# Optimization experiments

Hardware: AMD Instinct MI355X
Metric: run time of the kernel (lower is better)

The kernel has to match this reference:

```python
import jax, jax.numpy as jnp
import numpy as np

TOP_K = 4

def setup_inputs() -> dict:
    key = jax.random.key(0)
    ks = jax.random.split(key, 10)
    s = 0.02
    return {
        "x": jax.random.normal(ks[0], (4, 1024, 2048), jnp.float32),
        "expert_bias": jnp.zeros((64,), jnp.float32),
        "router_w": jax.random.normal(ks[1], (64, 2048), jnp.float32) * s,
        "gate_w": jax.random.normal(ks[2], (8192, 2048), jnp.float32) * s,
        "up_w": jax.random.normal(ks[3], (8192, 2048), jnp.float32) * s,
        "down_w": jax.random.normal(ks[4], (2048, 8192), jnp.float32) * s,
        "w_down": jax.random.normal(ks[5], (512, 2048), jnp.float32) * s,
        "w_up": jax.random.normal(ks[6], (2048, 512), jnp.float32) * s,
        "experts_w12": jax.random.normal(ks[7], (64, 512, 2048), jnp.float32) * s,
        "experts_w3": jax.random.normal(ks[8], (64, 1024, 512), jnp.float32) * s,
    }


def reference(x, expert_bias, router_w, gate_w, up_w, down_w, w_down, w_up, experts_w12, experts_w3):
    B, S, D = x.shape
    E = router_w.shape[0]
    K = TOP_K
    h = x.reshape(-1, D)            # [N, D]
    N = h.shape[0]
    NK = N * K

    # --- router (fp32) ---
    logits = h @ router_w.T          # [N, E]
    scores = jax.nn.sigmoid(logits)
    z_loss = jnp.mean(logits * logits) * 1e-4
    sel = scores + expert_bias
    _, topk_idx = jax.lax.top_k(sel, K)                      # [N, K]
    topk_logits = jnp.take_along_axis(logits, topk_idx, axis=1)
    gating = jax.nn.softmax(topk_logits, axis=-1)            # [N, K]

    # --- shared SwiGLU expert ---
    shared = (jax.nn.silu(h @ gate_w.T) * (h @ up_w.T)) @ down_w.T   # [N, D]

    # --- bottleneck down projection ---
    hd = h @ w_down.T                # [N, bottle]
    Bn = hd.shape[1]

    # --- dispatch: sort tokens by expert, capacity max_load per expert ---
    flat = topk_idx.reshape(-1)                      # [NK]
    perm = jnp.argsort(flat)                         # stable sort
    sorted_e = flat[perm]
    counts = jnp.bincount(flat, length=E)
    ptr = jnp.cumsum(counts) - counts                # start offset per expert
    local = jnp.arange(NK) - ptr[sorted_e]           # rank within expert
    max_load = (NK // E // 8 + 6) * 8                # static python int
    num_slots = E * max_load
    mask = local < max_load
    slots = sorted_e * max_load + local
    tok = jnp.repeat(jnp.arange(N), K)               # token id per routed slot

    # reverse_map[slot] = token index (N = dummy)
    rm = jnp.full((num_slots + 1,), N, dtype=jnp.int32)
    rm = rm.at[jnp.where(mask, slots, num_slots)].set(tok[perm].astype(jnp.int32))
    reverse_map = rm[:num_slots]

    hwd = jnp.concatenate([hd, jnp.zeros((1, Bn), hd.dtype)], axis=0)
    padding = hwd[reverse_map].reshape(E, max_load, Bn)

    # --- grouped expert GEMMs ---
    h12 = jnp.einsum('emb,ebf->emf', padding, experts_w12)   # [E, L, 2*F]
    h1, h2 = jnp.split(h12, 2, axis=-1)
    pout = jnp.einsum('emf,efb->emb', jax.nn.silu(h1) * h2, experts_w3)
    pout = pout.reshape(-1, Bn)                              # [num_slots, bottle]

    # --- combine: gather back per (token, k) slot and mix with gating ---
    powd = jnp.concatenate([pout, jnp.zeros((1, Bn), pout.dtype)], axis=0)
    gm = jnp.full((NK + 1,), num_slots, dtype=jnp.int32)
    gm = gm.at[jnp.where(mask, perm, NK)].set(jnp.where(mask, slots, num_slots).astype(jnp.int32))
    gather_map = gm[:NK]
    gathered = powd[gather_map].reshape(N, K, Bn)
    routed_b = jnp.einsum('nk,nkb->nb', gating, gathered)
    routed = routed_b @ w_up.T                               # [N, D]

    # eval mode: route_scale = 1.0, moe_scale = 0.5 (one shared expert), aux_loss = 0
    out = (shared + routed) * 0.5
    return out.reshape(B, S, D), z_loss
```

## Files before the change

### kernel.cpp

```cpp
#include <hip/hip_runtime.h>
#include <math.h>

#define NTOK 4096
#define DMODEL 2048
#define ENUM 64
#define HSH 8192
#define BND 512
#define FEXP 1024
#define MAXL 304
#define EPAD 384
#define ECH 16

typedef float f32x4 __attribute__((ext_vector_type(4)));
using bf16x8 = __attribute__((ext_vector_type(8))) __bf16;

typedef const __attribute__((address_space(1))) unsigned int cgu32;
typedef __attribute__((address_space(3))) unsigned int lu32;
#define GLOAD16(g, l) __builtin_amdgcn_global_load_lds((cgu32*)(g), (lu32*)(l), 16, 0, 0)

__device__ __forceinline__ unsigned short f2bf(float f) {
    union { float f; unsigned int u; } v; v.f = f;
    unsigned int u = v.u;
    return (unsigned short)((u + 0x7FFFu + ((u >> 16) & 1u)) >> 16);
}
__device__ __forceinline__ float bf2f(unsigned short s) {
    union { unsigned int u; float f; } v; v.u = ((unsigned int)s) << 16;
    return v.f;
}

__global__ __launch_bounds__(256) void init_kernel(float* zacc, int* slot2tok, unsigned short* hdz) {
    int i = blockIdx.x * 256 + threadIdx.x;
    if (i == 0) *zacc = 0.f;
    if (i < ENUM * MAXL) slot2tok[i] = NTOK;
    if (i < BND) hdz[i] = 0;
}

__global__ __launch_bounds__(256) void convert_kernel(
    const float* __restrict__ in, unsigned short* __restrict__ out, long long n)
{
    long long stride = (long long)gridDim.x * 256 * 8;
    for (long long i = ((long long)blockIdx.x * 256 + threadIdx.x) * 8; i < n; i += stride) {
        float4 a = *(const float4*)(in + i);
        float4 b = *(const float4*)(in + i + 4);
        union { unsigned short s[8]; uint4 v; } o;
        o.s[0] = f2bf(a.x); o.s[1] = f2bf(a.y); o.s[2] = f2bf(a.z); o.s[3] = f2bf(a.w);
        o.s[4] = f2bf(b.x); o.s[5] = f2bf(b.y); o.s[6] = f2bf(b.z); o.s[7] = f2bf(b.w);
        *(uint4*)(out + i) = o.v;
    }
}

__global__ __launch_bounds__(256) void convert_x_kernel(
    const float* __restrict__ in, unsigned short* __restrict__ hi,
    unsigned short* __restrict__ lo, long long n)
{
    long long stride = (long long)gridDim.x * 256 * 8;
    for (long long i = ((long long)blockIdx.x * 256 + threadIdx.x) * 8; i < n; i += stride) {
        float4 a = *(const float4*)(in + i);
        float4 b = *(const float4*)(in + i + 4);
        union { unsigned short s[8]; uint4 v; } oh, ol;
        float f[8] = {a.x, a.y, a.z, a.w, b.x, b.y, b.z, b.w};
#pragma unroll
        for (int j = 0; j < 8; j++) {
            unsigned short h = f2bf(f[j]);
            oh.s[j] = h;
            ol.s[j] = f2bf(f[j] - bf2f(h));
        }
        *(uint4*)(hi + i) = oh.v;
        *(uint4*)(lo + i) = ol.v;
    }
}

__global__ __launch_bounds__(256) void convert_rw_kernel(
    const float* __restrict__ rw, unsigned short* __restrict__ whi,
    unsigned short* __restrict__ wlo)
{
    int i = (blockIdx.x * 256 + threadIdx.x) * 4;
    if (i >= 128 * 2048) return;
    ushort4 oh = {0, 0, 0, 0}, ol = {0, 0, 0, 0};
    if (i < 64 * 2048) {
        float4 f = *(const float4*)(rw + i);
        float v[4] = {f.x, f.y, f.z, f.w};
        unsigned short h;
        h = f2bf(v[0]); oh.x = h; ol.x = f2bf(v[0] - bf2f(h));
        h = f2bf(v[1]); oh.y = h; ol.y = f2bf(v[1] - bf2f(h));
        h = f2bf(v[2]); oh.z = h; ol.z = f2bf(v[2] - bf2f(h));
        h = f2bf(v[3]); oh.w = h; ol.w = f2bf(v[3] - bf2f(h));
    }
    *(ushort4*)(whi + i) = oh;
    *(ushort4*)(wlo + i) = ol;
}

__global__ __launch_bounds__(256) void tconv_kernel(
    const float* __restrict__ in, unsigned short* __restrict__ out, int Kd, int Nd)
{
    __shared__ float t[32][33];
    size_t zoff = (size_t)blockIdx.z * Kd * Nd;
    in += zoff; out += zoff;
    int n0 = blockIdx.x * 32, k0 = blockIdx.y * 32;
    int r = threadIdx.x >> 3, c = (threadIdx.x & 7) * 4;
    float4 v = *(const float4*)(in + (size_t)(k0 + r) * Nd + n0 + c);
    t[r][c] = v.x; t[r][c + 1] = v.y; t[r][c + 2] = v.z; t[r][c + 3] = v.w;
    __syncthreads();
    ushort4 o;
    o.x = f2bf(t[c + 0][r]); o.y = f2bf(t[c + 1][r]);
    o.z = f2bf(t[c + 2][r]); o.w = f2bf(t[c + 3][r]);
    *(ushort4*)(out + (size_t)(n0 + r) * Kd + k0 + c) = o;
}

__global__ __launch_bounds__(256) void rgemm_kernel(
    const unsigned short* __restrict__ xb, const unsigned short* __restrict__ xlo,
    const unsigned short* __restrict__ whi, const unsigned short* __restrict__ wlo,
    float* __restrict__ logits)
{
    __shared__ unsigned short As[2][128 * 64];
    __shared__ unsigned short Bs[2][128 * 64];
    const int z = blockIdx.z;
    const int m0 = blockIdx.y * 128;
    const int tid = threadIdx.x;
    const int lane = tid & 63;
    const int w = tid >> 6;
    const int wm = (w >> 1) * 64;
    const int wn = (w & 1) * 64;

    const unsigned short* Ab = (z == 2) ? xlo : xb;
    const unsigned short* Bb = (z == 1) ? wlo : whi;
    float* Cb = logits + (size_t)z * NTOK * 128;

    size_t asrc[4], bsrc[4];
    int ldso[4];
#pragma unroll
    for (int i = 0; i < 4; i++) {
        int u = i * 256 + tid;
        int r = u >> 3;
        int ce = ((u & 7) ^ (r & 7)) * 8;
        ldso[i] = u * 8;
        asrc[i] = (size_t)(m0 + r) * DMODEL + ce;
        bsrc[i] = (size_t)r * DMODEL + ce;
    }

    const int lrow = lane & 15;
    const int kg = lane >> 4;
    const int mk = (lrow & 7) << 4;
    int arx[4], brx[4];
#pragma unroll
    for (int t = 0; t < 4; t++) {
        arx[t] = (wm + t * 16 + lrow) * 128;
        brx[t] = (wn + t * 16 + lrow) * 128;
    }

    f32x4 acc[4][4];
#pragma unroll
    for (int a = 0; a < 4; a++)
#pragma unroll
        for (int b = 0; b < 4; b++) acc[a][b] = (f32x4)0.f;

#pragma unroll
    for (int i = 0; i < 4; i++) GLOAD16(Ab + asrc[i], &As[0][ldso[i]]);
#pragma unroll
    for (int i = 0; i < 4; i++) GLOAD16(Bb + bsrc[i], &Bs[0][ldso[i]]);
#pragma unroll
    for (int i = 0; i < 4; i++) GLOAD16(Ab + asrc[i] + 64, &As[1][ldso[i]]);
#pragma unroll
    for (int i = 0; i < 4; i++) GLOAD16(Bb + bsrc[i] + 64, &Bs[1][ldso[i]]);

    const int nt = DMODEL >> 6;
    int cur = 0;
    for (int t = 0; t < nt; ++t) {
        if (t + 1 < nt) asm volatile("s_waitcnt vmcnt(8)" ::: "memory");
        else            asm volatile("s_waitcnt vmcnt(0)" ::: "memory");
        __builtin_amdgcn_s_barrier();
        __builtin_amdgcn_sched_barrier(0);
        const char* Abase = (const char*)&As[cur][0];
        const char* Bbase = (const char*)&Bs[cur][0];
#pragma unroll
        for (int ks = 0; ks < 2; ks++) {
            const int cb = (ks * 64 + kg * 16) ^ mk;
            bf16x8 a[4], b[4];
#pragma unroll
            for (int t2 = 0; t2 < 4; t2++) {
                a[t2] = *(const bf16x8*)(Abase + arx[t2] + cb);
                b[t2] = *(const bf16x8*)(Bbase + brx[t2] + cb);
            }
#pragma unroll
            for (int ni = 0; ni < 4; ni++)
#pragma unroll
                for (int mi = 0; mi < 4; mi++)
                    acc[mi][ni] = __builtin_amdgcn_mfma_f32_16x16x32_bf16(a[mi], b[ni], acc[mi][ni], 0, 0, 0);
        }
        __builtin_amdgcn_sched_barrier(0);
        asm volatile("s_waitcnt lgkmcnt(0)" ::: "memory");
        __builtin_amdgcn_s_barrier();
        __builtin_amdgcn_sched_barrier(0);
        const int kn = (t + 2) * 64;
        if (kn < DMODEL) {
#pragma unroll
            for (int i = 0; i < 4; i++) GLOAD16(Ab + asrc[i] + kn, &As[cur][ldso[i]]);
#pragma unroll
            for (int i = 0; i < 4; i++) GLOAD16(Bb + bsrc[i] + kn, &Bs[cur][ldso[i]]);
        }
        cur ^= 1;
    }

    const int rb0 = m0 + wm + (kg << 2);
#pragma unroll
    for (int mi = 0; mi < 4; mi++)
#pragma unroll
        for (int ni = 0; ni < 4; ni++) {
            int col = wn + ni * 16 + lrow;
#pragma unroll
            for (int r = 0; r < 4; r++)
                Cb[(size_t)(rb0 + mi * 16 + r) * 128 + col] = acc[mi][ni][r];
        }
}

__global__ __launch_bounds__(256) void topk_kernel(
    const float* __restrict__ logits, const float* __restrict__ bias,
    int* __restrict__ topk_idx, float* __restrict__ gating, float* __restrict__ zacc)
{
    __shared__ float zpart[4];
    const size_t Z = (size_t)NTOK * 128;
    int wv = threadIdx.x >> 6, lane = threadIdx.x & 63;
    int n = blockIdx.x * 4 + wv;
    const float* lp = logits + (size_t)n * 128 + lane;
    float logit = lp[0] + lp[Z] + lp[2 * Z];
    float sel = 1.f / (1.f + expf(-logit)) + bias[lane];
    float zsq = logit * logit;
    for (int off = 32; off; off >>= 1) zsq += __shfl_down(zsq, off);
    if (lane == 0) zpart[wv] = zsq;
    __syncthreads();
    if (threadIdx.x == 0) atomicAdd(zacc, zpart[0] + zpart[1] + zpart[2] + zpart[3]);
    float cur = sel;
    float ch_logit[4]; int ch_idx[4];
    for (int kk = 0; kk < 4; kk++) {
        float v = cur; int idx = lane;
        for (int off = 1; off < 64; off <<= 1) {
            float v2 = __shfl_xor(v, off);
            int i2 = __shfl_xor(idx, off);
            if (v2 > v || (v2 == v && i2 < idx)) { v = v2; idx = i2; }
        }
        ch_idx[kk] = idx;
        ch_logit[kk] = __shfl(logit, idx);
        if (lane == idx) cur = -1e30f;
    }
    if (lane == 0) {
        float mx = ch_logit[0];
        for (int kk = 1; kk < 4; kk++) mx = fmaxf(mx, ch_logit[kk]);
        float se = 0.f, ex[4];
        for (int kk = 0; kk < 4; kk++) { ex[kk] = expf(ch_logit[kk] - mx); se += ex[kk]; }
        for (int kk = 0; kk < 4; kk++) {
            topk_idx[n * 4 + kk] = ch_idx[kk];
            gating[n * 4 + kk] = ex[kk] / se;
        }
    }
}

__global__ __launch_bounds__(256) void rank_kernel(
    const int* __restrict__ topk_idx, int* __restrict__ slot2tok, int* __restrict__ gmap)
{
    int e = blockIdx.x;
    __shared__ int wsum[4];
    int tid = threadIdx.x;
    int lane = tid & 63, w = tid >> 6;
    int running = 0;
    for (int c = 0; c < NTOK * 4; c += 256) {
        int i = c + tid;
        int fl = topk_idx[i];
        bool m = (fl == e);
        unsigned long long bal = __ballot(m);
        int prefix = __popcll(bal & ((1ULL << lane) - 1ULL));
        if (lane == 0) wsum[w] = __popcll(bal);
        __syncthreads();
        int wbase = 0;
        for (int j = 0; j < w; j++) wbase += wsum[j];
        int total = wsum[0] + wsum[1] + wsum[2] + wsum[3];
        if (m) {
            int rank = running + wbase + prefix;
            int tok = i >> 2;
            if (rank < MAXL) {
                slot2tok[e * MAXL + rank] = tok;
                gmap[i] = e * MAXL + rank;
            } else gmap[i] = -1;
        }
        running += total;
        __syncthreads();
    }
}

template<int GATHER, int EPI>
__global__ __launch_bounds__(256) void gemm2(
    const unsigned short* __restrict__ A, long long aZ, int lda,
    const int* __restrict__ gtab,
    const unsigned short* __restrict__ Bm, long long bZ, int ldb,
    void* __restrict__ Cb, long long cZ, int ldc,
    int M, int K)
{
    __shared__ unsigned short As[2][128 * 64];
    __shared__ unsigned short Bs[2][128 * 64];
    const int z = blockIdx.z;
    const int m0 = blockIdx.y * 128;
    const int n0 = blockIdx.x * 128;
    const int tid = threadIdx.x;
    const int lane = tid & 63;
    const int w = tid >> 6;
    const int wm = (w >> 1) * 64;
    const int wn = (w & 1) * 64;

    const unsigned short* Ab = A + (GATHER ? (size_t)0 : (size_t)z * aZ);
    const unsigned short* Bb = Bm + (size_t)z * bZ;

    size_t asrc[4], bsrc[4];
    int ldso[4];
#pragma unroll
    for (int i = 0; i < 4; i++) {
        int u = i * 256 + tid;
        int r = u >> 3;
        int ce = ((u & 7) ^ (r & 7)) * 8;
        ldso[i] = u * 8;
        if constexpr (GATHER) {
            int mr = m0 + r;
            int tok = (mr < M) ? gtab[(size_t)z * MAXL + mr] : NTOK;
            asrc[i] = (size_t)tok * lda + ce;
        } else {
            asrc[i] = (size_t)(m0 + r) * lda + ce;
        }
        bsrc[i] = (size_t)(n0 + r) * ldb + ce;
    }

    const int lrow = lane & 15;
    const int kg = lane >> 4;
    const int mk = (lrow & 7) << 4;
    int arx[4], brx[4];
#pragma unroll
    for (int t = 0; t < 4; t++) {
        arx[t] = (wm + t * 16 + lrow) * 128;
        brx[t] = (wn + t * 16 + lrow) * 128;
    }

    f32x4 acc[4][4];
#pragma unroll
    for (int a = 0; a < 4; a++)
#pragma unroll
        for (int b = 0; b < 4; b++) acc[a][b] = (f32x4)0.f;

#pragma unroll
    for (int i = 0; i < 4; i++) GLOAD16(Ab + asrc[i], &As[0][ldso[i]]);
#pragma unroll
    for (int i = 0; i < 4; i++) GLOAD16(Bb + bsrc[i], &Bs[0][ldso[i]]);
    if (64 < K) {
#pragma unroll
        for (int i = 0; i < 4; i++) GLOAD16(Ab + asrc[i] + 64, &As[1][ldso[i]]);
#pragma unroll
        for (int i = 0; i < 4; i++) GLOAD16(Bb + bsrc[i] + 64, &Bs[1][ldso[i]]);
    }

    const int nt = K >> 6;
    int cur = 0;
    for (int t = 0; t < nt; ++t) {
        if (t + 1 < nt) asm volatile("s_waitcnt vmcnt(8)" ::: "memory");
        else            asm volatile("s_waitcnt vmcnt(0)" ::: "memory");
        __builtin_amdgcn_s_barrier();
        __builtin_amdgcn_sched_barrier(0);
        const char* Abase = (const char*)&As[cur][0];
        const char* Bbase = (const char*)&Bs[cur][0];
#pragma unroll
        for (int ks = 0; ks < 2; ks++) {
            const int cb = (ks * 64 + kg * 16) ^ mk;
            bf16x8 a[4], b[4];
#pragma unroll
            for (int t2 = 0; t2 < 4; t2++) {
                a[t2] = *(const bf16x8*)(Abase + arx[t2] + cb);
                b[t2] = *(const bf16x8*)(Bbase + brx[t2] + cb);
            }
#pragma unroll
            for (int ni = 0; ni < 4; ni++)
#pragma unroll
                for (int mi = 0; mi < 4; mi++)
                    acc[mi][ni] = __builtin_amdgcn_mfma_f32_16x16x32_bf16(a[mi], b[ni], acc[mi][ni], 0, 0, 0);
        }
        __builtin_amdgcn_sched_barrier(0);
        asm volatile("s_waitcnt lgkmcnt(0)" ::: "memory");
        __builtin_amdgcn_s_barrier();
        __builtin_amdgcn_sched_barrier(0);
        const int kn = (t + 2) * 64;
        if (kn < K) {
#pragma unroll
            for (int i = 0; i < 4; i++) GLOAD16(Ab + asrc[i] + kn, &As[cur][ldso[i]]);
#pragma unroll
            for (int i = 0; i < 4; i++) GLOAD16(Bb + bsrc[i] + kn, &Bs[cur][ldso[i]]);
        }
        cur ^= 1;
    }

    const int rb0 = m0 + wm + (kg << 2);
#pragma unroll
    for (int mi = 0; mi < 4; mi++)
#pragma unroll
        for (int ni = 0; ni < 4; ni++) {
            int col = n0 + wn + ni * 16 + lrow;
#pragma unroll
            for (int r = 0; r < 4; r++) {
                int row = rb0 + mi * 16 + r;
                if (row < M) {
                    size_t ci = (size_t)z * cZ + (size_t)row * ldc + col;
                    float v = acc[mi][ni][r];
                    if constexpr (EPI == 0) {
                        ((unsigned short*)Cb)[ci] = f2bf(v);
                    } else if constexpr (EPI == 1) {
                        unsigned short* cp = (unsigned short*)Cb + ci;
                        float g = bf2f(*cp);
                        *cp = f2bf(g / (1.f + expf(-g)) * v);
                    } else if constexpr (EPI == 2) {
                        ((float*)Cb)[ci] = v;
                    } else {
                        float* cp = (float*)Cb + ci;
                        *cp = (*cp + v) * 0.5f;
                    }
                }
            }
        }
}

template<int EPI>
__global__ __launch_bounds__(512) void gemm3(
    const unsigned short* __restrict__ A, int lda,
    const unsigned short* __restrict__ Bm, int ldb,
    unsigned short* __restrict__ C, int ldc, int K)
{
    __shared__ unsigned short As[3][256 * 32];
    __shared__ unsigned short Bs[3][256 * 32];
    const int m0 = blockIdx.y * 256;
    const int n0 = blockIdx.x * 256;
    const int tid = threadIdx.x;
    const int lane = tid & 63;
    const int w = tid >> 6;
    const int wm = (w >> 2) * 128;
    const int wn = (w & 3) * 64;

    size_t asrc[2], bsrc[2];
    int ldso[2];
#pragma unroll
    for (int i = 0; i < 2; i++) {
        int u = i * 512 + tid;
        int r = u >> 2;
        int ce = ((u & 3) ^ ((r >> 1) & 3)) * 8;
        ldso[i] = u * 8;
        asrc[i] = (size_t)(m0 + r) * lda + ce;
        bsrc[i] = (size_t)(n0 + r) * ldb + ce;
    }

    const int lrow = lane & 15;
    const int kg = lane >> 4;
    const int un = (kg ^ ((lrow >> 1) & 3)) << 4;
    int arx[8], brx[4];
#pragma unroll
    for (int mi = 0; mi < 8; mi++) arx[mi] = (wm + mi * 16 + lrow) * 64 + un;
#pragma unroll
    for (int ni = 0; ni < 4; ni++) brx[ni] = (wn + ni * 16 + lrow) * 64 + un;

    f32x4 acc[8][4];
#pragma unroll
    for (int a = 0; a < 8; a++)
#pragma unroll
        for (int b = 0; b < 4; b++) acc[a][b] = (f32x4)0.f;

#pragma unroll
    for (int i = 0; i < 2; i++) GLOAD16(A + asrc[i], &As[0][ldso[i]]);
#pragma unroll
    for (int i = 0; i < 2; i++) GLOAD16(Bm + bsrc[i], &Bs[0][ldso[i]]);
#pragma unroll
    for (int i = 0; i < 2; i++) GLOAD16(A + asrc[i] + 32, &As[1][ldso[i]]);
#pragma unroll
    for (int i = 0; i < 2; i++) GLOAD16(Bm + bsrc[i] + 32, &Bs[1][ldso[i]]);

    const int nt = K >> 5;
    int cur = 0;
    for (int t = 0; t < nt; ++t) {
        if (t + 1 < nt) asm volatile("s_waitcnt vmcnt(4)" ::: "memory");
        else            asm volatile("s_waitcnt vmcnt(0)" ::: "memory");
        __builtin_amdgcn_s_barrier();
        __builtin_amdgcn_sched_barrier(0);
        if (t + 2 < nt) {
            int nb = cur + 2; if (nb >= 3) nb -= 3;
            const int kn = (t + 2) * 32;
#pragma unroll
            for (int i = 0; i < 2; i++) GLOAD16(A + asrc[i] + kn, &As[nb][ldso[i]]);
#pragma unroll
            for (int i = 0; i < 2; i++) GLOAD16(Bm + bsrc[i] + kn, &Bs[nb][ldso[i]]);
        }
        const char* Abase = (const char*)&As[cur][0];
        const char* Bbase = (const char*)&Bs[cur][0];
        bf16x8 a[8], b[4];
#pragma unroll
        for (int mi = 0; mi < 8; mi++) a[mi] = *(const bf16x8*)(Abase + arx[mi]);
#pragma unroll
        for (int ni = 0; ni < 4; ni++) b[ni] = *(const bf16x8*)(Bbase + brx[ni]);
        __builtin_amdgcn_s_setprio(1);
#pragma unroll
        for (int ni = 0; ni < 4; ni++)
#pragma unroll
            for (int mi = 0; mi < 8; mi++)
                acc[mi][ni] = __builtin_amdgcn_mfma_f32_16x16x32_bf16(a[mi], b[ni], acc[mi][ni], 0, 0, 0);
        __builtin_amdgcn_s_setprio(0);
        __builtin_amdgcn_sched_barrier(0);
        asm volatile("s_waitcnt lgkmcnt(0)" ::: "memory");
        __builtin_amdgcn_s_barrier();
        __builtin_amdgcn_sched_barrier(0);
        cur += 1; if (cur >= 3) cur -= 3;
    }

    const int rb0 = m0 + wm + (kg << 2);
#pragma unroll
    for (int mi = 0; mi < 8; mi++)
#pragma unroll
        for (int ni = 0; ni < 4; ni++) {
            int col = n0 + wn + ni * 16 + lrow;
#pragma unroll
            for (int r = 0; r < 4; r++) {
                int row = rb0 + mi * 16 + r;
                size_t ci = (size_t)row * ldc + col;
                float v = acc[mi][ni][r];
                if constexpr (EPI == 0) {
                    C[ci] = f2bf(v);
                } else {
                    unsigned short* cp = C + ci;
                    float g = bf2f(*cp);
                    *cp = f2bf(g / (1.f + expf(-g)) * v);
                }
            }
        }
}

__global__ __launch_bounds__(256) void siluact_kernel(
    const unsigned short* __restrict__ h12, unsigned short* __restrict__ act)
{
    int e = blockIdx.y, m = blockIdx.x;
    const unsigned short* hr = h12 + ((size_t)e * EPAD + m) * 2048;
    unsigned short* ar = act + ((size_t)e * EPAD + m) * 1024;
    int j = threadIdx.x * 4;
    ushort4 h1 = *(const ushort4*)(hr + j);
    ushort4 h2 = *(const ushort4*)(hr + 1024 + j);
    ushort4 o;
    float v;
    v = bf2f(h1.x); o.x = f2bf(v / (1.f + expf(-v)) * bf2f(h2.x));
    v = bf2f(h1.y); o.y = f2bf(v / (1.f + expf(-v)) * bf2f(h2.y));
    v = bf2f(h1.z); o.z = f2bf(v / (1.f + expf(-v)) * bf2f(h2.z));
    v = bf2f(h1.w); o.w = f2bf(v / (1.f + expf(-v)) * bf2f(h2.w));
    *(ushort4*)(ar + j) = o;
}

__global__ __launch_bounds__(256) void gather_kernel(
    const unsigned short* __restrict__ pout, const int* __restrict__ gmap,
    const float* __restrict__ gating, unsigned short* __restrict__ routed_b)
{
    int n = blockIdx.x;
    int j = threadIdx.x * 2;
    float a0 = 0.f, a1 = 0.f;
#pragma unroll
    for (int kk = 0; kk < 4; kk++) {
        int slot = gmap[n * 4 + kk];
        float g = gating[n * 4 + kk];
        if (slot >= 0) {
            const unsigned short* pr = pout + (size_t)slot * BND + j;
            a0 += g * bf2f(pr[0]);
            a1 += g * bf2f(pr[1]);
        }
    }
    routed_b[(size_t)n * BND + j] = f2bf(a0);
    routed_b[(size_t)n * BND + j + 1] = f2bf(a1);
}

__global__ void zloss_kernel(const float* zacc, float* out) {
    out[0] = zacc[0] * (1.0e-4f / (float)(NTOK * ENUM));
}

extern "C" void kernel_launch(void* const* d_in, const int* in_sizes, int n_in,
                              void* d_out, int out_size, void* d_ws, size_t ws_size,
                              hipStream_t stream)
{
    const float* x      = (const float*)d_in[0];
    const float* ebias  = (const float*)d_in[1];
    const float* rw     = (const float*)d_in[2];
    const float* gate_w = (const float*)d_in[3];
    const float* up_w   = (const float*)d_in[4];
    const float* down_w = (const float*)d_in[5];
    const float* w_down = (const float*)d_in[6];
    const float* w_up   = (const float*)d_in[7];
    const float* w12    = (const float*)d_in[8];
    const float* w3     = (const float*)d_in[9];
    float* out = (float*)d_out;

    char* ws = (char*)d_ws;
    size_t off = 0;
    auto alloc = [&](size_t b) { size_t o = off; off += (b + 255) & ~(size_t)255; return o; };
    float* zacc     = (float*)(ws + alloc(4));
    int*   topk     = (int*)(ws + alloc((size_t)NTOK * 4 * 4));
    float* gating   = (float*)(ws + alloc((size_t)NTOK * 4 * 4));
    int*   gmap     = (int*)(ws + alloc((size_t)NTOK * 4 * 4));
    int*   slot2tok = (int*)(ws + alloc((size_t)ENUM * MAXL * 4));
    unsigned short* xb     = (unsigned short*)(ws + alloc((size_t)NTOK * DMODEL * 2));
    unsigned short* hd     = (unsigned short*)(ws + alloc((size_t)(NTOK + 1) * BND * 2));
    unsigned short* rb     = (unsigned short*)(ws + alloc((size_t)NTOK * BND * 2));
    unsigned short* wdownb = (unsigned short*)(ws + alloc((size_t)BND * DMODEL * 2));
    unsigned short* wupb   = (unsigned short*)(ws + alloc((size_t)DMODEL * BND * 2));
    unsigned short* wbuf   = (unsigned short*)(ws + alloc((size_t)HSH * DMODEL * 2));
    unsigned short* H1     = (unsigned short*)(ws + alloc((size_t)NTOK * HSH * 2));
    unsigned short* h12  = H1;
    unsigned short* act  = H1 + (size_t)ECH * EPAD * 2048;
    unsigned short* pout = H1 + (size_t)ECH * EPAD * 2048 + (size_t)ECH * EPAD * 1024;
    unsigned short* xlo    = H1;
    float*          logits = (float*)((char*)H1 + (size_t)NTOK * DMODEL * 2);
    unsigned short* whi    = (unsigned short*)((char*)logits + (size_t)3 * NTOK * 128 * 4);
    unsigned short* wlo    = whi + (size_t)128 * DMODEL;

    init_kernel<<<(ENUM * MAXL + 255) / 256, 256, 0, stream>>>(zacc, slot2tok, hd + (size_t)NTOK * BND);

    convert_x_kernel<<<1024, 256, 0, stream>>>(x, xb, xlo, (long long)NTOK * DMODEL);
    convert_rw_kernel<<<(128 * 2048 / 4 + 255) / 256, 256, 0, stream>>>(rw, whi, wlo);
    rgemm_kernel<<<dim3(1, NTOK / 128, 3), 256, 0, stream>>>(xb, xlo, whi, wlo, logits);
    topk_kernel<<<NTOK / 4, 256, 0, stream>>>(logits, ebias, topk, gating, zacc);
    rank_kernel<<<ENUM, 256, 0, stream>>>(topk, slot2tok, gmap);

    convert_kernel<<<256, 256, 0, stream>>>(w_down, wdownb, (long long)BND * DMODEL);
    convert_kernel<<<256, 256, 0, stream>>>(w_up, wupb, (long long)DMODEL * BND);

    gemm2<0, 0><<<dim3(BND / 128, NTOK / 128, 1), 256, 0, stream>>>(
        xb, 0, DMODEL, nullptr, wdownb, 0, DMODEL, hd, 0, BND, NTOK, DMODEL);

    convert_kernel<<<1024, 256, 0, stream>>>(gate_w, wbuf, (long long)HSH * DMODEL);
    gemm3<0><<<dim3(HSH / 256, NTOK / 256), 512, 0, stream>>>(
        xb, DMODEL, wbuf, DMODEL, H1, HSH, DMODEL);
    convert_kernel<<<1024, 256, 0, stream>>>(up_w, wbuf, (long long)HSH * DMODEL);
    gemm3<1><<<dim3(HSH / 256, NTOK / 256), 512, 0, stream>>>(
        xb, DMODEL, wbuf, DMODEL, H1, HSH, DMODEL);
    convert_kernel<<<1024, 256, 0, stream>>>(down_w, wbuf, (long long)DMODEL * HSH);
    gemm2<0, 2><<<dim3(DMODEL / 128, NTOK / 128, 1), 256, 0, stream>>>(
        H1, 0, HSH, nullptr, wbuf, 0, HSH, out, 0, DMODEL, NTOK, HSH);

    for (int c = 0; c < ENUM / ECH; c++) {
        tconv_kernel<<<dim3(2048 / 32, 512 / 32, ECH), 256, 0, stream>>>(
            w12 + (size_t)c * ECH * 512 * 2048, wbuf, 512, 2048);
        gemm2<1, 0><<<dim3(2048 / 128, 3, ECH), 256, 0, stream>>>(
            hd, 0, BND, slot2tok + (size_t)c * ECH * MAXL,
            wbuf, (long long)2048 * 512, 512,
            h12, (long long)EPAD * 2048, 2048, MAXL, BND);
        tconv_kernel<<<dim3(512 / 32, 1024 / 32, ECH), 256, 0, stream>>>(
            w3 + (size_t)c * ECH * 1024 * 512, wbuf, 1024, 512);
        siluact_kernel<<<dim3(EPAD, ECH), 256, 0, stream>>>(h12, act);
        gemm2<0, 0><<<dim3(BND / 128, 3, ECH), 256, 0, stream>>>(
            act, (long long)EPAD * FEXP, FEXP, nullptr,
            wbuf, (long long)BND * FEXP, FEXP,
            pout + (size_t)c * ECH * MAXL * BND, (long long)MAXL * BND, BND, MAXL, FEXP);
    }

    gather_kernel<<<NTOK, 256, 0, stream>>>(pout, gmap, gating, rb);

    gemm2<0, 3><<<dim3(DMODEL / 128, NTOK / 128, 1), 256, 0, stream>>>(
        rb, 0, BND, nullptr, wupb, 0, BND, out, 0, DMODEL, NTOK, BND);

    zloss_kernel<<<1, 1, 0, stream>>>(zacc, out + (size_t)NTOK * DMODEL);
}
```

Baseline: 1.124 ms.

## Deepen shared-GEMM pipeline to 4 stages and interleave prefetch with MFMA phases

The 256x256 bf16 GEMM used for the shared expert's gate and up projections moves from a 3-buffer to a 4-buffer LDS ring, prefetching three K-tiles ahead. The second end-of-iteration barrier is removed, and the A fragment loads and global prefetches are split into four phases that are interleaved with the MFMA groups. The aim is to hide global-load latency and shorten barrier stalls. In exchange, LDS use per block grows to 128KB, which limits occupancy to one block per CU. There is also a possible WAR hazard, because prefetches into slot (kt+3)&3 now rely on only one barrier per iteration.

```diff
diff --git a/kernel.cpp b/kernel.cpp
--- a/kernel.cpp
+++ b/kernel.cpp
@@ -421,13 +421,13 @@
 }
 
 template<int EPI>
-__global__ __launch_bounds__(512) void gemm3(
+__global__ __launch_bounds__(512) void gemm4(
     const unsigned short* __restrict__ A, int lda,
     const unsigned short* __restrict__ Bm, int ldb,
     unsigned short* __restrict__ C, int ldc, int K)
 {
-    __shared__ unsigned short As[3][256 * 32];
-    __shared__ unsigned short Bs[3][256 * 32];
+    __shared__ unsigned short As[4][256 * 32];
+    __shared__ unsigned short Bs[4][256 * 32];
     const int m0 = blockIdx.y * 256;
     const int n0 = blockIdx.x * 256;
     const int tid = threadIdx.x;
@@ -463,49 +463,54 @@
 #pragma unroll
         for (int b = 0; b < 4; b++) acc[a][b] = (f32x4)0.f;
 
-#pragma unroll
-    for (int i = 0; i < 2; i++) GLOAD16(A + asrc[i], &As[0][ldso[i]]);
-#pragma unroll
-    for (int i = 0; i < 2; i++) GLOAD16(Bm + bsrc[i], &Bs[0][ldso[i]]);
-#pragma unroll
-    for (int i = 0; i < 2; i++) GLOAD16(A + asrc[i] + 32, &As[1][ldso[i]]);
-#pragma unroll
-    for (int i = 0; i < 2; i++) GLOAD16(Bm + bsrc[i] + 32, &Bs[1][ldso[i]]);
-
-    const int nt = K >> 5;
-    int cur = 0;
-    for (int t = 0; t < nt; ++t) {
-        if (t + 1 < nt) asm volatile("s_waitcnt vmcnt(4)" ::: "memory");
-        else            asm volatile("s_waitcnt vmcnt(0)" ::: "memory");
+    const int NT = K >> 5;
+    for (int t = 0; t < 3 && t < NT; ++t) {
+        const int kn = t * 32;
+        GLOAD16(A + asrc[0] + kn, &As[t][ldso[0]]);
+        GLOAD16(A + asrc[1] + kn, &As[t][ldso[1]]);
+        GLOAD16(Bm + bsrc[0] + kn, &Bs[t][ldso[0]]);
+        GLOAD16(Bm + bsrc[1] + kn, &Bs[t][ldso[1]]);
+    }
+
+    for (int kt = 0; kt < NT; ++kt) {
+        if (kt < NT - 2)       asm volatile("s_waitcnt vmcnt(8)" ::: "memory");
+        else if (kt == NT - 2) asm volatile("s_waitcnt vmcnt(4)" ::: "memory");
+        else                   asm volatile("s_waitcnt vmcnt(0)" ::: "memory");
         __builtin_amdgcn_s_barrier();
         __builtin_amdgcn_sched_barrier(0);
-        if (t + 2 < nt) {
-            int nb = cur + 2; if (nb >= 3) nb -= 3;
-            const int kn = (t + 2) * 32;
-#pragma unroll
-            for (int i = 0; i < 2; i++) GLOAD16(A + asrc[i] + kn, &As[nb][ldso[i]]);
-#pragma unroll
-            for (int i = 0; i < 2; i++) GLOAD16(Bm + bsrc[i] + kn, &Bs[nb][ldso[i]]);
-        }
-        const char* Abase = (const char*)&As[cur][0];
-        const char* Bbase = (const char*)&Bs[cur][0];
-        bf16x8 a[8], b[4];
-#pragma unroll
-        for (int mi = 0; mi < 8; mi++) a[mi] = *(const bf16x8*)(Abase + arx[mi]);
-#pragma unroll
-        for (int ni = 0; ni < 4; ni++) b[ni] = *(const bf16x8*)(Bbase + brx[ni]);
-        __builtin_amdgcn_s_setprio(1);
-#pragma unroll
-        for (int ni = 0; ni < 4; ni++)
-#pragma unroll
-            for (int mi = 0; mi < 8; mi++)
-                acc[mi][ni] = __builtin_amdgcn_mfma_f32_16x16x32_bf16(a[mi], b[ni], acc[mi][ni], 0, 0, 0);
-        __builtin_amdgcn_s_setprio(0);
-        __builtin_amdgcn_sched_barrier(0);
-        asm volatile("s_waitcnt lgkmcnt(0)" ::: "memory");
-        __builtin_amdgcn_s_barrier();
-        __builtin_amdgcn_sched_barrier(0);
-        cur += 1; if (cur >= 3) cur -= 3;
+
+        const char* Ab = (const char*)&As[kt & 3][0];
+        const char* Bb = (const char*)&Bs[kt & 3][0];
+        const bool pf = (kt + 3 < NT);
+        const int slot = (kt + 3) & 3;
+        const int kn = (kt + 3) * 32;
+
+        bf16x8 b[4];
+#pragma unroll
+        for (int ni = 0; ni < 4; ni++) b[ni] = *(const bf16x8*)(Bb + brx[ni]);
+
+#define G4_PHASE(q, GL)                                                              \
+        {                                                                            \
+            bf16x8 a0 = *(const bf16x8*)(Ab + arx[2 * (q)]);                         \
+            bf16x8 a1 = *(const bf16x8*)(Ab + arx[2 * (q) + 1]);                     \
+            GL;                                                                      \
+            __builtin_amdgcn_s_setprio(1);                                           \
+            _Pragma("unroll")                                                        \
+            for (int ni = 0; ni < 4; ni++) {                                         \
+                acc[2 * (q)][ni] = __builtin_amdgcn_mfma_f32_16x16x32_bf16(          \
+                    a0, b[ni], acc[2 * (q)][ni], 0, 0, 0);                           \
+                acc[2 * (q) + 1][ni] = __builtin_amdgcn_mfma_f32_16x16x32_bf16(      \
+                    a1, b[ni], acc[2 * (q) + 1][ni], 0, 0, 0);                       \
+            }                                                                        \
+            __builtin_amdgcn_s_setprio(0);                                           \
+            __builtin_amdgcn_sched_barrier(0);                                       \
+        }
+
+        G4_PHASE(0, if (pf) GLOAD16(A + asrc[0] + kn, &As[slot][ldso[0]]))
+        G4_PHASE(1, if (pf) GLOAD16(A + asrc[1] + kn, &As[slot][ldso[1]]))
+        G4_PHASE(2, if (pf) GLOAD16(Bm + bsrc[0] + kn, &Bs[slot][ldso[0]]))
+        G4_PHASE(3, if (pf) GLOAD16(Bm + bsrc[1] + kn, &Bs[slot][ldso[1]]))
+#undef G4_PHASE
     }
 
     const int rb0 = m0 + wm + (kg << 2);
@@ -627,10 +632,10 @@
         xb, 0, DMODEL, nullptr, wdownb, 0, DMODEL, hd, 0, BND, NTOK, DMODEL);
 
     convert_kernel<<<1024, 256, 0, stream>>>(gate_w, wbuf, (long long)HSH * DMODEL);
-    gemm3<0><<<dim3(HSH / 256, NTOK / 256), 512, 0, stream>>>(
+    gemm4<0><<<dim3(HSH / 256, NTOK / 256), 512, 0, stream>>>(
         xb, DMODEL, wbuf, DMODEL, H1, HSH, DMODEL);
     convert_kernel<<<1024, 256, 0, stream>>>(up_w, wbuf, (long long)HSH * DMODEL);
-    gemm3<1><<<dim3(HSH / 256, NTOK / 256), 512, 0, stream>>>(
+    gemm4<1><<<dim3(HSH / 256, NTOK / 256), 512, 0, stream>>>(
         xb, DMODEL, wbuf, DMODEL, H1, HSH, DMODEL);
     convert_kernel<<<1024, 256, 0, stream>>>(down_w, wbuf, (long long)DMODEL * HSH);
     gemm2<0, 2><<<dim3(DMODEL / 128, NTOK / 128, 1), 256, 0, stream>>>(
```

After: 1.078 ms. 1.04x faster.
